# Kernel optimization log

Hardware: AMD Instinct MI355X
Metric: run time of the kernel (lower is better)

## Reference

```python
import jax, jax.numpy as jnp
import numpy as np


def _forward_algorithm(emissions, mask, start, end, trans, reverse):
    """emissions: (B, L, T), mask: (B, L) -> log probs (L, B, T)."""
    em = jnp.transpose(emissions, (1, 0, 2))          # (L, B, T)
    m = jnp.transpose(mask.astype(em.dtype), (1, 0))  # (L, B)
    B, T = em.shape[1], em.shape[2]
    if not reverse:
        init = em[0] + start[None, :]                 # (B, T)

        def step(prev, xs):
            e_t, m_t = xs
            # inner[b, j, k] = prev[b, j] + trans[j, k] + em_t[b, k]
            inner = prev[:, :, None] + trans[None, :, :] + e_t[:, None, :]
            new = jax.nn.logsumexp(inner, axis=1)
            new = new * m_t[:, None] + prev * (1.0 - m_t)[:, None]
            return new, new

        _, ys = jax.lax.scan(step, init, (em[1:], m[1:]))
        return jnp.concatenate([init[None], ys], axis=0)
    else:
        init = jnp.broadcast_to(end[None, :], (B, T))
        transT = trans.T

        def step(prev, xs):
            e_t, m_t = xs
            # inner[b, j, k] = prev[b, j] + trans[k, j] + em_t[b, j]
            inner = prev[:, :, None] + transT[None, :, :] + e_t[:, :, None]
            new = jax.nn.logsumexp(inner, axis=1)
            new = new * m_t[:, None] + prev * (1.0 - m_t)[:, None]
            return new, new

        # iterate i = L-1 ... 1 (reverse), result index i-1
        _, ys = jax.lax.scan(step, init, (em[1:][::-1], m[1:][::-1]))
        return jnp.concatenate([ys[::-1], init[None]], axis=0)


def setup_inputs() -> dict:
    key = jax.random.key(0)
    k1, k2, k3, k4 = jax.random.split(key, 4)
    B, L, T = 256, 1024, 64
    emissions = jax.random.normal(k1, (B, L, T), dtype=jnp.float32)
    start_transitions = jax.random.normal(k2, (T,), dtype=jnp.float32)
    end_transitions = jax.random.normal(k3, (T,), dtype=jnp.float32)
    transitions = jax.random.normal(k4, (T, T), dtype=jnp.float32)
    mask = jnp.ones((B, L), dtype=jnp.int32)
    return {
        "emissions": emissions,
        "start_transitions": start_transitions,
        "end_transitions": end_transitions,
        "transitions": transitions,
        "mask": mask,
    }


def reference(emissions, start_transitions, end_transitions, transitions, mask):
    """CRF marginal probabilities. Returns (seq_len, batch, num_tags)."""
    alpha = _forward_algorithm(emissions, mask, start_transitions,
                               end_transitions, transitions, reverse=False)
    beta = _forward_algorithm(emissions, mask, start_transitions,
                              end_transitions, transitions, reverse=True)
    z = jax.nn.logsumexp(alpha[-1] + end_transitions[None, :], axis=1)  # (B,)
    return jnp.exp(alpha + beta - z[None, :, None])
```

## Files before the change

kernel.cpp:

```cpp
#include <hip/hip_runtime.h>

#define B_ 256
#define L_ 1024
#define T_ 64

typedef float f4v __attribute__((ext_vector_type(4)));

__device__ __forceinline__ float rfl(float x) {
    return __int_as_float(__builtin_amdgcn_readfirstlane(__float_as_int(x)));
}
__device__ __forceinline__ float rlane(float x, int j) {
    return __int_as_float(__builtin_amdgcn_readlane(__float_as_int(x), j));
}

__global__ __launch_bounds__(64, 1)
void crf_scan(const float* __restrict__ em, const float* __restrict__ start_t,
              const float* __restrict__ end_t, const float* __restrict__ trans,
              const int* __restrict__ mask, float* __restrict__ alpha,
              float* __restrict__ beta, float* __restrict__ zbuf)
{
    const int lane = threadIdx.x;
    const int cb = blockIdx.x;
    const bool fwd = cb < B_;
    const int b = fwd ? cb : cb - B_;

    float e[T_];
    if (fwd) {
#pragma unroll
        for (int j = 0; j < T_; ++j) e[j] = __expf(trans[j * T_ + lane]);
    } else {
#pragma unroll
        for (int j = 0; j < T_; ++j) e[j] = __expf(trans[lane * T_ + j]);
    }

    const float* emb = em + (size_t)b * (L_ * T_);
    const int* mb = mask + (size_t)b * L_;
    const size_t stride = (size_t)B_ * T_;

    if (fwd) {
        float st0 = emb[lane] + start_t[lane];
        float c = rfl(st0);
        float u = __expf(st0 - c);
        float* ap = alpha + (size_t)b * T_ + lane;
        *ap = st0;
        ap += stride;

        float pe0 = emb[1 * T_ + lane], pe1 = emb[2 * T_ + lane],
              pe2 = emb[3 * T_ + lane], pe3 = emb[4 * T_ + lane],
              pe4 = emb[5 * T_ + lane], pe5 = emb[6 * T_ + lane];
        int pm0 = mb[1], pm1 = mb[2], pm2 = mb[3], pm3 = mb[4],
            pm4 = mb[5], pm5 = mb[6];

        for (int t = 1; t < L_; ++t) {
            float f = __expf(pe0);
            int mv = pm0;
            pe0 = pe1; pe1 = pe2; pe2 = pe3; pe3 = pe4; pe4 = pe5;
            pm0 = pm1; pm1 = pm2; pm2 = pm3; pm3 = pm4; pm4 = pm5;
            int tn = t + 6; if (tn > L_ - 1) tn = L_ - 1;
            pe5 = emb[(size_t)tn * T_ + lane];
            pm5 = mb[tn];

            float um = u;
            float acc[4] = {0.f, 0.f, 0.f, 0.f};
#pragma unroll
            for (int j = 0; j < 32; ++j) {
                float uj = rlane(u, j);
                acc[j & 3] = fmaf(uj, e[j], acc[j & 3]);
            }
#pragma unroll
            for (int j = 32; j < 64; ++j) {
                float uj = rlane(u, j);
                acc[j & 3] = fmaf(uj, e[j], acc[j & 3]);
            }
            float dot = (acc[0] + acc[1]) + (acc[2] + acc[3]);
            float d0 = rfl(dot);
            float f0 = rfl(f);
            float u00 = d0 * f0;
            float r = __builtin_amdgcn_rcpf(u00);
            float cand = (dot * f) * r;
            float cn = c + __logf(u00);
            float un = (mv != 0) ? cand : um;
            c = (mv != 0) ? cn : c;
            float av = c + __logf(un);
            *ap = av;
            ap += stride;
            u = un;
        }
        float v = u * __expf(end_t[lane]);
        for (int off = 32; off; off >>= 1) v += __shfl_xor(v, off);
        if (lane == 0) zbuf[b] = c + __logf(v);
    } else {
        float bv0 = end_t[lane];
        float c = rfl(bv0);
        float u = __expf(bv0 - c);
        float* bp = beta + ((size_t)(L_ - 1) * B_ + b) * T_ + lane;
        *bp = bv0;
        bp -= stride;

        float pe0 = emb[(size_t)(L_ - 1) * T_ + lane], pe1 = emb[(size_t)(L_ - 2) * T_ + lane],
              pe2 = emb[(size_t)(L_ - 3) * T_ + lane], pe3 = emb[(size_t)(L_ - 4) * T_ + lane],
              pe4 = emb[(size_t)(L_ - 5) * T_ + lane], pe5 = emb[(size_t)(L_ - 6) * T_ + lane];
        int pm0 = mb[L_ - 1], pm1 = mb[L_ - 2], pm2 = mb[L_ - 3],
            pm3 = mb[L_ - 4], pm4 = mb[L_ - 5], pm5 = mb[L_ - 6];

        for (int i = L_ - 1; i >= 1; --i) {
            float f = __expf(pe0);
            int mv = pm0;
            pe0 = pe1; pe1 = pe2; pe2 = pe3; pe3 = pe4; pe4 = pe5;
            pm0 = pm1; pm1 = pm2; pm2 = pm3; pm3 = pm4; pm4 = pm5;
            int tn = i - 6; if (tn < 1) tn = 1;
            pe5 = emb[(size_t)tn * T_ + lane];
            pm5 = mb[tn];

            float w = u * f;
            float um = u;
            float acc[4] = {0.f, 0.f, 0.f, 0.f};
#pragma unroll
            for (int j = 0; j < 32; ++j) {
                float wj = rlane(w, j);
                acc[j & 3] = fmaf(wj, e[j], acc[j & 3]);
            }
#pragma unroll
            for (int j = 32; j < 64; ++j) {
                float wj = rlane(w, j);
                acc[j & 3] = fmaf(wj, e[j], acc[j & 3]);
            }
            float dot = (acc[0] + acc[1]) + (acc[2] + acc[3]);
            float u00 = rfl(dot);
            float r = __builtin_amdgcn_rcpf(u00);
            float cand = dot * r;
            float cn = c + __logf(u00);
            float un = (mv != 0) ? cand : um;
            c = (mv != 0) ? cn : c;
            float bvv = c + __logf(un);
            *bp = bvv;
            bp -= stride;
            u = un;
        }
    }
}

__global__ __launch_bounds__(256)
void crf_finalize(const float* __restrict__ alpha,
                  const float* __restrict__ zbuf,
                  float* __restrict__ out)
{
    size_t i4 = (size_t)blockIdx.x * blockDim.x + threadIdx.x;
    const f4v* a4 = (const f4v*)alpha;
    f4v* o4 = (f4v*)out;
    int b = (int)((i4 >> 4) & (B_ - 1));
    float z = zbuf[b];
    f4v a = a4[i4];
    f4v bb = o4[i4];
    f4v o;
    o.x = __expf(a.x + bb.x - z);
    o.y = __expf(a.y + bb.y - z);
    o.z = __expf(a.z + bb.z - z);
    o.w = __expf(a.w + bb.w - z);
    __builtin_nontemporal_store(o, &o4[i4]);
}

extern "C" void kernel_launch(void* const* d_in, const int* in_sizes, int n_in,
                              void* d_out, int out_size, void* d_ws, size_t ws_size,
                              hipStream_t stream) {
    const float* em = (const float*)d_in[0];
    const float* st = (const float*)d_in[1];
    const float* en = (const float*)d_in[2];
    const float* tr = (const float*)d_in[3];
    const int*   mk = (const int*)d_in[4];
    float* out   = (float*)d_out;
    float* alpha = (float*)d_ws;
    float* zbuf  = alpha + (size_t)L_ * B_ * T_;

    crf_scan<<<2 * B_, T_, 0, stream>>>(em, st, en, tr, mk, alpha, out, zbuf);
    size_t n4 = (size_t)L_ * B_ * T_ / 4;
    crf_finalize<<<(int)(n4 / 256), 256, 0, stream>>>(alpha, zbuf, out);
}
```

Baseline: 531.7 us.

## Replace readlane broadcast dot product with DPP row-rotate dual-chain accumulation

The per-step 64-term matrix-vector dot product no longer broadcasts each lane's value through scalar readlane. It rotates the state vector across lanes with DPP row-rotate in two opposite directions, and the transition weights are pre-permuted to match the rotation order. Emission prefetch depth goes from 6 to 8 steps, and the finalize kernel now has each thread handle 8 vec4 elements over a fixed 2048-block grid. The intent is to remove the scalar readlane round-trips and their latency from the serial recurrence. It relies on the DPP rotation pattern exactly covering all 64 lanes, which is fragile if row_ror only rotates within 16-lane rows.

```diff
diff --git a/kernel.cpp b/kernel.cpp
--- a/kernel.cpp
+++ b/kernel.cpp
@@ -9,9 +9,22 @@
 __device__ __forceinline__ float rfl(float x) {
     return __int_as_float(__builtin_amdgcn_readfirstlane(__float_as_int(x)));
 }
-__device__ __forceinline__ float rlane(float x, int j) {
-    return __int_as_float(__builtin_amdgcn_readlane(__float_as_int(x), j));
-}
+__device__ __forceinline__ int roti(int i) {
+    return __builtin_amdgcn_update_dpp(i, i, 0x134, 0xF, 0xF, false);
+}
+__device__ __forceinline__ int rori(int i) {
+    return __builtin_amdgcn_update_dpp(i, i, 0x13C, 0xF, 0xF, false);
+}
+__device__ __forceinline__ float rotf(float x) {
+    return __int_as_float(roti(__float_as_int(x)));
+}
+__device__ __forceinline__ float rorf(float x) {
+    return __int_as_float(rori(__float_as_int(x)));
+}
+
+#define REP32(M) M(0) M(1) M(2) M(3) M(4) M(5) M(6) M(7) M(8) M(9) M(10) M(11) \
+    M(12) M(13) M(14) M(15) M(16) M(17) M(18) M(19) M(20) M(21) M(22) M(23) \
+    M(24) M(25) M(26) M(27) M(28) M(29) M(30) M(31)
 
 __global__ __launch_bounds__(64, 1)
 void crf_scan(const float* __restrict__ em, const float* __restrict__ start_t,
@@ -24,18 +37,35 @@
     const bool fwd = cb < B_;
     const int b = fwd ? cb : cb - B_;
 
-    float e[T_];
-    if (fwd) {
-#pragma unroll
-        for (int j = 0; j < T_; ++j) e[j] = __expf(trans[j * T_ + lane]);
-    } else {
-#pragma unroll
-        for (int j = 0; j < T_; ++j) e[j] = __expf(trans[lane * T_ + j]);
+#define DECL_E(s) float eA##s, eB##s;
+    REP32(DECL_E)
+#undef DECL_E
+
+    {
+        int idxA = lane;
+        int idxB = lane;
+        if (fwd) {
+#define GF(s) eA##s = __expf(trans[idxA * T_ + lane]); idxA = roti(idxA); \
+              idxB = rori(idxB); eB##s = __expf(trans[idxB * T_ + lane]);
+            REP32(GF)
+#undef GF
+        } else {
+#define GB(s) eA##s = __expf(trans[lane * T_ + idxA]); idxA = roti(idxA); \
+              idxB = rori(idxB); eB##s = __expf(trans[lane * T_ + idxB]);
+            REP32(GB)
+#undef GB
+        }
     }
+#define PIN(s) asm volatile("" : "+v"(eA##s), "+v"(eB##s));
+    REP32(PIN)
+#undef PIN
 
     const float* emb = em + (size_t)b * (L_ * T_);
     const int* mb = mask + (size_t)b * L_;
     const size_t stride = (size_t)B_ * T_;
+
+#define DOT(s) accA = fmaf(uA, eA##s, accA); uA = rotf(uA); \
+               uB = rorf(uB);                accB = fmaf(uB, eB##s, accB);
 
     if (fwd) {
         float st0 = emb[lane] + start_t[lane];
@@ -47,39 +77,34 @@
 
         float pe0 = emb[1 * T_ + lane], pe1 = emb[2 * T_ + lane],
               pe2 = emb[3 * T_ + lane], pe3 = emb[4 * T_ + lane],
-              pe4 = emb[5 * T_ + lane], pe5 = emb[6 * T_ + lane];
+              pe4 = emb[5 * T_ + lane], pe5 = emb[6 * T_ + lane],
+              pe6 = emb[7 * T_ + lane], pe7 = emb[8 * T_ + lane];
         int pm0 = mb[1], pm1 = mb[2], pm2 = mb[3], pm3 = mb[4],
-            pm4 = mb[5], pm5 = mb[6];
+            pm4 = mb[5], pm5 = mb[6], pm6 = mb[7], pm7 = mb[8];
 
         for (int t = 1; t < L_; ++t) {
             float f = __expf(pe0);
             int mv = pm0;
-            pe0 = pe1; pe1 = pe2; pe2 = pe3; pe3 = pe4; pe4 = pe5;
-            pm0 = pm1; pm1 = pm2; pm2 = pm3; pm3 = pm4; pm4 = pm5;
-            int tn = t + 6; if (tn > L_ - 1) tn = L_ - 1;
-            pe5 = emb[(size_t)tn * T_ + lane];
-            pm5 = mb[tn];
-
-            float um = u;
-            float acc[4] = {0.f, 0.f, 0.f, 0.f};
-#pragma unroll
-            for (int j = 0; j < 32; ++j) {
-                float uj = rlane(u, j);
-                acc[j & 3] = fmaf(uj, e[j], acc[j & 3]);
-            }
-#pragma unroll
-            for (int j = 32; j < 64; ++j) {
-                float uj = rlane(u, j);
-                acc[j & 3] = fmaf(uj, e[j], acc[j & 3]);
-            }
-            float dot = (acc[0] + acc[1]) + (acc[2] + acc[3]);
+            pe0 = pe1; pe1 = pe2; pe2 = pe3; pe3 = pe4;
+            pe4 = pe5; pe5 = pe6; pe6 = pe7;
+            pm0 = pm1; pm1 = pm2; pm2 = pm3; pm3 = pm4;
+            pm4 = pm5; pm5 = pm6; pm6 = pm7;
+            int tn = t + 8; if (tn > L_ - 1) tn = L_ - 1;
+            pe7 = emb[(size_t)tn * T_ + lane];
+            pm7 = mb[tn];
+
+            float uA = u, uB = u;
+            float accA = 0.f, accB = 0.f;
+            REP32(DOT)
+            float dot = accA + accB;
+
+            float f0 = rfl(f);
             float d0 = rfl(dot);
-            float f0 = rfl(f);
             float u00 = d0 * f0;
             float r = __builtin_amdgcn_rcpf(u00);
             float cand = (dot * f) * r;
             float cn = c + __logf(u00);
-            float un = (mv != 0) ? cand : um;
+            float un = (mv != 0) ? cand : u;
             c = (mv != 0) ? cn : c;
             float av = c + __logf(un);
             *ap = av;
@@ -99,38 +124,34 @@
 
         float pe0 = emb[(size_t)(L_ - 1) * T_ + lane], pe1 = emb[(size_t)(L_ - 2) * T_ + lane],
               pe2 = emb[(size_t)(L_ - 3) * T_ + lane], pe3 = emb[(size_t)(L_ - 4) * T_ + lane],
-              pe4 = emb[(size_t)(L_ - 5) * T_ + lane], pe5 = emb[(size_t)(L_ - 6) * T_ + lane];
+              pe4 = emb[(size_t)(L_ - 5) * T_ + lane], pe5 = emb[(size_t)(L_ - 6) * T_ + lane],
+              pe6 = emb[(size_t)(L_ - 7) * T_ + lane], pe7 = emb[(size_t)(L_ - 8) * T_ + lane];
         int pm0 = mb[L_ - 1], pm1 = mb[L_ - 2], pm2 = mb[L_ - 3],
-            pm3 = mb[L_ - 4], pm4 = mb[L_ - 5], pm5 = mb[L_ - 6];
+            pm3 = mb[L_ - 4], pm4 = mb[L_ - 5], pm5 = mb[L_ - 6],
+            pm6 = mb[L_ - 7], pm7 = mb[L_ - 8];
 
         for (int i = L_ - 1; i >= 1; --i) {
             float f = __expf(pe0);
             int mv = pm0;
-            pe0 = pe1; pe1 = pe2; pe2 = pe3; pe3 = pe4; pe4 = pe5;
-            pm0 = pm1; pm1 = pm2; pm2 = pm3; pm3 = pm4; pm4 = pm5;
-            int tn = i - 6; if (tn < 1) tn = 1;
-            pe5 = emb[(size_t)tn * T_ + lane];
-            pm5 = mb[tn];
+            pe0 = pe1; pe1 = pe2; pe2 = pe3; pe3 = pe4;
+            pe4 = pe5; pe5 = pe6; pe6 = pe7;
+            pm0 = pm1; pm1 = pm2; pm2 = pm3; pm3 = pm4;
+            pm4 = pm5; pm5 = pm6; pm6 = pm7;
+            int tn = i - 8; if (tn < 1) tn = 1;
+            pe7 = emb[(size_t)tn * T_ + lane];
+            pm7 = mb[tn];
 
             float w = u * f;
-            float um = u;
-            float acc[4] = {0.f, 0.f, 0.f, 0.f};
-#pragma unroll
-            for (int j = 0; j < 32; ++j) {
-                float wj = rlane(w, j);
-                acc[j & 3] = fmaf(wj, e[j], acc[j & 3]);
-            }
-#pragma unroll
-            for (int j = 32; j < 64; ++j) {
-                float wj = rlane(w, j);
-                acc[j & 3] = fmaf(wj, e[j], acc[j & 3]);
-            }
-            float dot = (acc[0] + acc[1]) + (acc[2] + acc[3]);
+            float uA = w, uB = w;
+            float accA = 0.f, accB = 0.f;
+            REP32(DOT)
+            float dot = accA + accB;
+
             float u00 = rfl(dot);
             float r = __builtin_amdgcn_rcpf(u00);
             float cand = dot * r;
             float cn = c + __logf(u00);
-            float un = (mv != 0) ? cand : um;
+            float un = (mv != 0) ? cand : u;
             c = (mv != 0) ? cn : c;
             float bvv = c + __logf(un);
             *bp = bvv;
@@ -138,6 +159,7 @@
             u = un;
         }
     }
+#undef DOT
 }
 
 __global__ __launch_bounds__(256)
@@ -145,19 +167,24 @@
                   const float* __restrict__ zbuf,
                   float* __restrict__ out)
 {
-    size_t i4 = (size_t)blockIdx.x * blockDim.x + threadIdx.x;
     const f4v* a4 = (const f4v*)alpha;
     f4v* o4 = (f4v*)out;
-    int b = (int)((i4 >> 4) & (B_ - 1));
-    float z = zbuf[b];
-    f4v a = a4[i4];
-    f4v bb = o4[i4];
-    f4v o;
-    o.x = __expf(a.x + bb.x - z);
-    o.y = __expf(a.y + bb.y - z);
-    o.z = __expf(a.z + bb.z - z);
-    o.w = __expf(a.w + bb.w - z);
-    __builtin_nontemporal_store(o, &o4[i4]);
+    size_t base = (size_t)blockIdx.x * 256 + threadIdx.x;
+    const size_t step = (size_t)2048 * 256;
+#pragma unroll
+    for (int r = 0; r < 8; ++r) {
+        size_t i4 = base + (size_t)r * step;
+        int b = (int)((i4 >> 4) & (B_ - 1));
+        float z = zbuf[b];
+        f4v a = a4[i4];
+        f4v bb = o4[i4];
+        f4v o;
+        o.x = __expf(a.x + bb.x - z);
+        o.y = __expf(a.y + bb.y - z);
+        o.z = __expf(a.z + bb.z - z);
+        o.w = __expf(a.w + bb.w - z);
+        __builtin_nontemporal_store(o, &o4[i4]);
+    }
 }
 
 extern "C" void kernel_launch(void* const* d_in, const int* in_sizes, int n_in,
@@ -173,6 +200,5 @@
     float* zbuf  = alpha + (size_t)L_ * B_ * T_;
 
     crf_scan<<<2 * B_, T_, 0, stream>>>(em, st, en, tr, mk, alpha, out, zbuf);
-    size_t n4 = (size_t)L_ * B_ * T_ / 4;
-    crf_finalize<<<(int)(n4 / 256), 256, 0, stream>>>(alpha, zbuf, out);
-}
+    crf_finalize<<<2048, 256, 0, stream>>>(alpha, zbuf, out);
+}
```

New measurement: 615.4 us. 1.16x slower.

## Stage emissions and mask into LDS via async loads; shorten per-step log chain

Applied to the files above, without the earlier changes.

The scan kernel now copies emissions in double-buffered 16-step chunks, and the whole mask, into LDS using global_load_lds, gated by vmcnt waits. This replaces per-step global register prefetch. The recurrence is reformulated so the log output comes from log(dot) plus the emission rather than log of the normalized value, and the backward pass folds the emission into the vector before the dot. The dot uses 8 accumulators instead of 4. The finalize kernel uses fewer blocks with 8 elements per thread. Risks are fragile vmcnt accounting and changed numerics when masked steps occur.

```diff
diff --git a/kernel.cpp b/kernel.cpp
--- a/kernel.cpp
+++ b/kernel.cpp
@@ -1,4 +1,5 @@
 #include <hip/hip_runtime.h>
+#include <stdint.h>
 
 #define B_ 256
 #define L_ 1024
@@ -12,6 +13,42 @@
 __device__ __forceinline__ float rlane(float x, int j) {
     return __int_as_float(__builtin_amdgcn_readlane(__float_as_int(x), j));
 }
+
+typedef __attribute__((address_space(3))) uint32_t lds_u32;
+typedef __attribute__((address_space(1))) uint32_t glb_u32;
+__device__ __forceinline__ void gload16(const void* g, void* l) {
+    __builtin_amdgcn_global_load_lds((const glb_u32*)(uintptr_t)g,
+                                     (lds_u32*)(uintptr_t)l, 16, 0, 0);
+}
+
+#define X64(M) M(0) M(1) M(2) M(3) M(4) M(5) M(6) M(7) M(8) M(9) M(10) M(11) \
+  M(12) M(13) M(14) M(15) M(16) M(17) M(18) M(19) M(20) M(21) M(22) M(23) \
+  M(24) M(25) M(26) M(27) M(28) M(29) M(30) M(31) M(32) M(33) M(34) M(35) \
+  M(36) M(37) M(38) M(39) M(40) M(41) M(42) M(43) M(44) M(45) M(46) M(47) \
+  M(48) M(49) M(50) M(51) M(52) M(53) M(54) M(55) M(56) M(57) M(58) M(59) \
+  M(60) M(61) M(62) M(63)
+
+#define XR0(M) M(0) M(8) M(16) M(24) M(32) M(40) M(48) M(56)
+#define XR1(M) M(1) M(9) M(17) M(25) M(33) M(41) M(49) M(57)
+#define XR2(M) M(2) M(10) M(18) M(26) M(34) M(42) M(50) M(58)
+#define XR3(M) M(3) M(11) M(19) M(27) M(35) M(43) M(51) M(59)
+#define XR4(M) M(4) M(12) M(20) M(28) M(36) M(44) M(52) M(60)
+#define XR5(M) M(5) M(13) M(21) M(29) M(37) M(45) M(53) M(61)
+#define XR6(M) M(6) M(14) M(22) M(30) M(38) M(46) M(54) M(62)
+#define XR7(M) M(7) M(15) M(23) M(31) M(39) M(47) M(55) M(63)
+
+#define DE(n) float e##n;
+#define LEF(n) e##n = __expf(trans[(n) * T_ + lane]);
+#define LEB(n) e##n = __expf(trans[lane * T_ + (n)]);
+#define D0(n) a0 = fmaf(rlane(dsrc, n), e##n, a0);
+#define D1(n) a1 = fmaf(rlane(dsrc, n), e##n, a1);
+#define D2(n) a2 = fmaf(rlane(dsrc, n), e##n, a2);
+#define D3(n) a3 = fmaf(rlane(dsrc, n), e##n, a3);
+#define D4(n) a4 = fmaf(rlane(dsrc, n), e##n, a4);
+#define D5(n) a5 = fmaf(rlane(dsrc, n), e##n, a5);
+#define D6(n) a6 = fmaf(rlane(dsrc, n), e##n, a6);
+#define D7(n) a7 = fmaf(rlane(dsrc, n), e##n, a7);
+#define DOT_ALL() XR0(D0) XR1(D1) XR2(D2) XR3(D3) XR4(D4) XR5(D5) XR6(D6) XR7(D7)
 
 __global__ __launch_bounds__(64, 1)
 void crf_scan(const float* __restrict__ em, const float* __restrict__ start_t,
@@ -24,120 +61,113 @@
     const bool fwd = cb < B_;
     const int b = fwd ? cb : cb - B_;
 
-    float e[T_];
-    if (fwd) {
-#pragma unroll
-        for (int j = 0; j < T_; ++j) e[j] = __expf(trans[j * T_ + lane]);
-    } else {
-#pragma unroll
-        for (int j = 0; j < T_; ++j) e[j] = __expf(trans[lane * T_ + j]);
-    }
+    __shared__ float em_lds[32 * T_];
+    __shared__ int   mk_lds[L_];
 
     const float* emb = em + (size_t)b * (L_ * T_);
     const int* mb = mask + (size_t)b * L_;
     const size_t stride = (size_t)B_ * T_;
 
+#define STAGE(ch) { \
+    const char* gs = (const char*)emb + (size_t)(ch) * 4096; \
+    char* ls = (char*)em_lds + ((ch) & 1) * 4096; \
+    gload16(gs + lane * 16, ls); \
+    gload16(gs + 1024 + lane * 16, ls + 1024); \
+    gload16(gs + 2048 + lane * 16, ls + 2048); \
+    gload16(gs + 3072 + lane * 16, ls + 3072); }
+
+    {
+        const char* gm = (const char*)mb;
+        char* lm = (char*)mk_lds;
+        gload16(gm + lane * 16, lm);
+        gload16(gm + 1024 + lane * 16, lm + 1024);
+        gload16(gm + 2048 + lane * 16, lm + 2048);
+        gload16(gm + 3072 + lane * 16, lm + 3072);
+    }
+    if (fwd) { STAGE(0) STAGE(1) } else { STAGE(63) STAGE(62) }
+
+    X64(DE)
+    if (fwd) { X64(LEF) } else { X64(LEB) }
+
+    asm volatile("s_waitcnt vmcnt(0)" ::: "memory");
+
     if (fwd) {
-        float st0 = emb[lane] + start_t[lane];
+        float em0 = em_lds[lane];
+        float st0 = em0 + start_t[lane];
         float c = rfl(st0);
         float u = __expf(st0 - c);
+        float av = st0;
         float* ap = alpha + (size_t)b * T_ + lane;
-        *ap = st0;
+        *ap = av;
         ap += stride;
 
-        float pe0 = emb[1 * T_ + lane], pe1 = emb[2 * T_ + lane],
-              pe2 = emb[3 * T_ + lane], pe3 = emb[4 * T_ + lane],
-              pe4 = emb[5 * T_ + lane], pe5 = emb[6 * T_ + lane];
-        int pm0 = mb[1], pm1 = mb[2], pm2 = mb[3], pm3 = mb[4],
-            pm4 = mb[5], pm5 = mb[6];
-
+#pragma unroll 1
         for (int t = 1; t < L_; ++t) {
-            float f = __expf(pe0);
-            int mv = pm0;
-            pe0 = pe1; pe1 = pe2; pe2 = pe3; pe3 = pe4; pe4 = pe5;
-            pm0 = pm1; pm1 = pm2; pm2 = pm3; pm3 = pm4; pm4 = pm5;
-            int tn = t + 6; if (tn > L_ - 1) tn = L_ - 1;
-            pe5 = emb[(size_t)tn * T_ + lane];
-            pm5 = mb[tn];
-
-            float um = u;
-            float acc[4] = {0.f, 0.f, 0.f, 0.f};
-#pragma unroll
-            for (int j = 0; j < 32; ++j) {
-                float uj = rlane(u, j);
-                acc[j & 3] = fmaf(uj, e[j], acc[j & 3]);
+            if ((t & 15) == 0) {
+                asm volatile("s_waitcnt vmcnt(16)" ::: "memory");
+                int ch = t >> 4;
+                if (ch < 63) STAGE(ch + 1)
             }
-#pragma unroll
-            for (int j = 32; j < 64; ++j) {
-                float uj = rlane(u, j);
-                acc[j & 3] = fmaf(uj, e[j], acc[j & 3]);
-            }
-            float dot = (acc[0] + acc[1]) + (acc[2] + acc[3]);
-            float d0 = rfl(dot);
-            float f0 = rfl(f);
-            float u00 = d0 * f0;
+            float emv = em_lds[(t & 31) * T_ + lane];
+            int mvv = mk_lds[t];
+            float dsrc = u;
+            float a0=0.f,a1=0.f,a2=0.f,a3=0.f,a4=0.f,a5=0.f,a6=0.f,a7=0.f;
+            DOT_ALL()
+            float dot = ((a0+a1)+(a2+a3))+((a4+a5)+(a6+a7));
+            float f = __expf(emv);
+            float ld = __logf(dot);
+            float u00 = rfl(dot) * rfl(f);
             float r = __builtin_amdgcn_rcpf(u00);
             float cand = (dot * f) * r;
-            float cn = c + __logf(u00);
-            float un = (mv != 0) ? cand : um;
-            c = (mv != 0) ? cn : c;
-            float av = c + __logf(un);
+            bool mk = (mvv != 0);
+            av = mk ? ((c + ld) + emv) : av;
+            c  = mk ? (c + rfl(ld) + rfl(emv)) : c;
+            u  = mk ? cand : u;
             *ap = av;
             ap += stride;
-            u = un;
         }
         float v = u * __expf(end_t[lane]);
         for (int off = 32; off; off >>= 1) v += __shfl_xor(v, off);
         if (lane == 0) zbuf[b] = c + __logf(v);
     } else {
-        float bv0 = end_t[lane];
-        float c = rfl(bv0);
-        float u = __expf(bv0 - c);
+        float bv = end_t[lane];
         float* bp = beta + ((size_t)(L_ - 1) * B_ + b) * T_ + lane;
-        *bp = bv0;
+        *bp = bv;
         bp -= stride;
-
-        float pe0 = emb[(size_t)(L_ - 1) * T_ + lane], pe1 = emb[(size_t)(L_ - 2) * T_ + lane],
-              pe2 = emb[(size_t)(L_ - 3) * T_ + lane], pe3 = emb[(size_t)(L_ - 4) * T_ + lane],
-              pe4 = emb[(size_t)(L_ - 5) * T_ + lane], pe5 = emb[(size_t)(L_ - 6) * T_ + lane];
-        int pm0 = mb[L_ - 1], pm1 = mb[L_ - 2], pm2 = mb[L_ - 3],
-            pm3 = mb[L_ - 4], pm4 = mb[L_ - 5], pm5 = mb[L_ - 6];
-
+        float emQ = em_lds[31 * T_ + lane];
+        float g = rfl(bv + emQ);
+        float v = __expf((bv + emQ) - g);
+        float fold = __expf(emQ);
+
+#pragma unroll 1
         for (int i = L_ - 1; i >= 1; --i) {
-            float f = __expf(pe0);
-            int mv = pm0;
-            pe0 = pe1; pe1 = pe2; pe2 = pe3; pe3 = pe4; pe4 = pe5;
-            pm0 = pm1; pm1 = pm2; pm2 = pm3; pm3 = pm4; pm4 = pm5;
-            int tn = i - 6; if (tn < 1) tn = 1;
-            pe5 = emb[(size_t)tn * T_ + lane];
-            pm5 = mb[tn];
-
-            float w = u * f;
-            float um = u;
-            float acc[4] = {0.f, 0.f, 0.f, 0.f};
-#pragma unroll
-            for (int j = 0; j < 32; ++j) {
-                float wj = rlane(w, j);
-                acc[j & 3] = fmaf(wj, e[j], acc[j & 3]);
+            if ((i & 15) == 0) {
+                asm volatile("s_waitcnt vmcnt(16)" ::: "memory");
+                int ch = i >> 4;
+                if (ch >= 2) STAGE(ch - 2)
             }
-#pragma unroll
-            for (int j = 32; j < 64; ++j) {
-                float wj = rlane(w, j);
-                acc[j & 3] = fmaf(wj, e[j], acc[j & 3]);
-            }
-            float dot = (acc[0] + acc[1]) + (acc[2] + acc[3]);
-            float u00 = rfl(dot);
+            float emv = em_lds[((i - 1) & 31) * T_ + lane];
+            int mvv = mk_lds[i];
+            float dsrc = v;
+            float a0=0.f,a1=0.f,a2=0.f,a3=0.f,a4=0.f,a5=0.f,a6=0.f,a7=0.f;
+            DOT_ALL()
+            float dot = ((a0+a1)+(a2+a3))+((a4+a5)+(a6+a7));
+            float f = __expf(emv);
+            float ld = __logf(dot);
+            float u00 = rfl(dot) * rfl(f);
             float r = __builtin_amdgcn_rcpf(u00);
-            float cand = dot * r;
-            float cn = c + __logf(u00);
-            float un = (mv != 0) ? cand : um;
-            c = (mv != 0) ? cn : c;
-            float bvv = c + __logf(un);
-            *bp = bvv;
+            float vu = (dot * f) * r;
+            float vm = (v * f) * __builtin_amdgcn_rcpf(fold);
+            bool mk = (mvv != 0);
+            bv = mk ? (g + ld) : bv;
+            g  = mk ? (g + rfl(ld) + rfl(emv)) : g;
+            v  = mk ? vu : vm;
+            fold = f;
+            *bp = bv;
             bp -= stride;
-            u = un;
         }
     }
+#undef STAGE
 }
 
 __global__ __launch_bounds__(256)
@@ -145,19 +175,24 @@
                   const float* __restrict__ zbuf,
                   float* __restrict__ out)
 {
-    size_t i4 = (size_t)blockIdx.x * blockDim.x + threadIdx.x;
     const f4v* a4 = (const f4v*)alpha;
     f4v* o4 = (f4v*)out;
-    int b = (int)((i4 >> 4) & (B_ - 1));
-    float z = zbuf[b];
-    f4v a = a4[i4];
-    f4v bb = o4[i4];
-    f4v o;
-    o.x = __expf(a.x + bb.x - z);
-    o.y = __expf(a.y + bb.y - z);
-    o.z = __expf(a.z + bb.z - z);
-    o.w = __expf(a.w + bb.w - z);
-    __builtin_nontemporal_store(o, &o4[i4]);
+    size_t base = (size_t)blockIdx.x * 256 + threadIdx.x;
+    const size_t step = (size_t)2048 * 256;
+#pragma unroll
+    for (int r = 0; r < 8; ++r) {
+        size_t i4 = base + (size_t)r * step;
+        int b = (int)((i4 >> 4) & (B_ - 1));
+        float z = zbuf[b];
+        f4v a = a4[i4];
+        f4v bb = o4[i4];
+        f4v o;
+        o.x = __expf(a.x + bb.x - z);
+        o.y = __expf(a.y + bb.y - z);
+        o.z = __expf(a.z + bb.z - z);
+        o.w = __expf(a.w + bb.w - z);
+        __builtin_nontemporal_store(o, &o4[i4]);
+    }
 }
 
 extern "C" void kernel_launch(void* const* d_in, const int* in_sizes, int n_in,
@@ -173,6 +208,5 @@
     float* zbuf  = alpha + (size_t)L_ * B_ * T_;
 
     crf_scan<<<2 * B_, T_, 0, stream>>>(em, st, en, tr, mk, alpha, out, zbuf);
-    size_t n4 = (size_t)L_ * B_ * T_ / 4;
-    crf_finalize<<<(int)(n4 / 256), 256, 0, stream>>>(alpha, zbuf, out);
-}
+    crf_finalize<<<2048, 256, 0, stream>>>(alpha, zbuf, out);
+}
```

Result: slower. 735.6 us (+38.3%).
